# Optimization experiments

Hardware: AMD Instinct MI355X
Metric: run time of the kernel (lower is better)

Reference implementation:

```python
import jax, jax.numpy as jnp
import numpy as np

N = 1024          # nodes per atom and per input graph / barycenter
K = 8             # num_atoms
OT_LAYERS = 3     # proximal-point outer iterations inside fgwd
SINKHORN_LAYERS = 3
GWB_LAYERS = 2    # barycenter alternating-optimization iterations
PROX_BETA = 0.1   # proximal / entropic regularization strength
EPS = 1e-16


def fgwd(Gs, ps, Gb, pb):
    """Gromov-Wasserstein distance via proximal point + Sinkhorn.
    Gs:(ns,ns), ps:(ns,1), Gb:(nb,nb), pb:(nb,1). Returns (d, T) with T:(ns,nb).
    Square-loss GW cost: c(T) = f1(Gs) ps 1^T + 1 (f2(Gb) pb)^T - 2 Gs T Gb^T."""
    ns, nb = Gs.shape[0], Gb.shape[0]
    cost_st = ((Gs * Gs) @ ps) + ((Gb * Gb) @ pb).T  # (ns,1)+(1,nb) -> (ns,nb)
    T0 = ps @ pb.T  # independent-coupling init

    def ot_step(T, _):
        cost = cost_st - 2.0 * (Gs @ T @ Gb.T)
        kernel = jnp.exp(-cost / PROX_BETA) * T  # proximal-point kernel

        def sink(carry, _):
            a, b = carry
            b = pb / (kernel.T @ a + EPS)
            a = ps / (kernel @ b + EPS)
            return (a, b), None

        (a, b), _ = jax.lax.scan(sink, (ps, pb), None, length=SINKHORN_LAYERS)
        return (a * kernel) * b.T, None

    T, _ = jax.lax.scan(ot_step, T0, None, length=OT_LAYERS)
    cost = cost_st - 2.0 * (Gs @ T @ Gb.T)
    d = jnp.sum(cost * T)
    return d, T


def setup_inputs() -> dict:
    key = jax.random.key(0)
    k1, k2, k3 = jax.random.split(key, 3)
    Gm = jax.random.uniform(k1, (N, N), jnp.float32)          # input graph (sigmoid-range adjacency)
    pm = jnp.ones((N, 1), jnp.float32) / N                    # uniform node distribution
    atoms_presig = jax.random.normal(k2, (K, N, N), jnp.float32)  # pre-sigmoid atom params
    probs = jnp.ones((K, N, 1), jnp.float32) / N              # uniform atom distributions
    weights = jax.nn.softmax(jax.random.normal(k3, (K,), jnp.float32))  # output_weights
    return {"Gm": Gm, "pm": pm, "atoms_presig": atoms_presig, "probs": probs,
            "weights": weights}


def reference(Gm, pm, atoms_presig, probs, weights):
    Gk = jax.nn.sigmoid(atoms_presig)              # output_atoms: (K,N,N)
    G_bary, pb = Gm, pm                            # init_mode=0 -> barycenter init from input M
    fgwd_v = jax.vmap(fgwd, in_axes=(0, 0, None, None))
    denom = pb @ pb.T                              # pb pb^T normalizer
    for _ in range(GWB_LAYERS):
        _, trans = fgwd_v(Gk, probs, G_bary, pb)   # trans: (K,N,N)
        # comp_fgwb: sum_k w_k * T_k^T G_k T_k / (pb pb^T)
        GT = jnp.einsum('knm,kmj->knj', Gk, trans)
        G_bary = jnp.einsum('k,kni,knj->ij', weights, trans, GT) / denom
    d_fgw, _ = fgwd(Gm, pm, G_bary, pb)
    return d_fgw, G_bary
```

## Files before the change

### kernel.cpp

```cpp
#include <hip/hip_runtime.h>
#include <math.h>

#define N_   1024
#define K_   8
#define OTL  3
#define SKL  3
#define GWBL 2
#define INVB 10.0f
#define EPSV 1e-16f
#define INVN (1.0f / 1024.0f)
#define NN   ((size_t)N_ * N_)
#define KN   (K_ * N_)

typedef __attribute__((ext_vector_type(8))) short short8;
typedef __attribute__((ext_vector_type(4))) float f32x4;
typedef unsigned short bfu;

__device__ __forceinline__ float b2f(bfu u) {
    unsigned x = ((unsigned)u) << 16;
    return __builtin_bit_cast(float, x);
}
__device__ __forceinline__ bfu f2b(float f) {
    unsigned u = __builtin_bit_cast(unsigned, f);
    unsigned r = u + 0x7fffu + ((u >> 16) & 1u);
    return (bfu)(r >> 16);
}

template<int EPI>
__global__ __launch_bounds__(256, 2)
void bgemm_k(const bfu* __restrict__ A, const bfu* __restrict__ B,
             void* __restrict__ Cp, size_t sA, size_t sB, size_t sC,
             const float* __restrict__ rv, const float* __restrict__ cv,
             const float* __restrict__ wts, float* __restrict__ rs) {
    __shared__ bfu As[2][128 * 32];
    __shared__ bfu Bs[2][128 * 32];

    const int z  = blockIdx.x;
    const int bm = blockIdx.y * 128, bn = blockIdx.z * 128;
    const int tid = threadIdx.x;
    const int lane = tid & 63, wv = tid >> 6;
    const int wr = wv >> 1, wc = wv & 1;

    if (EPI == 0) {
        if (rs && blockIdx.y == 0 && blockIdx.z == 0) {
            const float4 zf = {0.f, 0.f, 0.f, 0.f};
            #pragma unroll
            for (int b = 0; b < 3; ++b)
                *(float4*)&rs[b * KN + z * N_ + tid * 4] = zf;
        }
    }

    const bfu* Az = A + (size_t)z * sA;
    const bfu* Bz = B + (size_t)z * sB;

    const int sr = tid >> 2;
    const int sk = (tid & 3) * 8;
    const int fr = lane & 15;
    const int ks = (lane >> 4) * 8;

    f32x4 acc[4][4];
    #pragma unroll
    for (int i = 0; i < 4; i++)
        #pragma unroll
        for (int j = 0; j < 4; j++) acc[i][j] = (f32x4)0.f;

    for (int k0 = 0; k0 < N_; k0 += 64) {
        __syncthreads();
        #pragma unroll
        for (int sg = 0; sg < 2; ++sg) {
            #pragma unroll
            for (int h = 0; h < 2; ++h) {
                const int row = sr + h * 64;
                const bfu* ga = Az + (size_t)(bm + row) * N_ + k0 + sg * 32 + sk;
                const bfu* gb = Bz + (size_t)(bn + row) * N_ + k0 + sg * 32 + sk;
                __builtin_amdgcn_global_load_lds(
                    (const __attribute__((address_space(1))) unsigned int*)ga,
                    (__attribute__((address_space(3))) unsigned int*)&As[sg][row * 32 + sk],
                    16, 0, 0);
                __builtin_amdgcn_global_load_lds(
                    (const __attribute__((address_space(1))) unsigned int*)gb,
                    (__attribute__((address_space(3))) unsigned int*)&Bs[sg][row * 32 + sk],
                    16, 0, 0);
            }
        }
        __syncthreads();

        #pragma unroll
        for (int sg = 0; sg < 2; ++sg) {
            short8 af[4], bf[4];
            #pragma unroll
            for (int mi = 0; mi < 4; ++mi)
                af[mi] = *(const short8*)&As[sg][(wr * 64 + mi * 16 + fr) * 32 + ks];
            #pragma unroll
            for (int ni = 0; ni < 4; ++ni)
                bf[ni] = *(const short8*)&Bs[sg][(wc * 64 + ni * 16 + fr) * 32 + ks];
            #pragma unroll
            for (int mi = 0; mi < 4; ++mi)
                #pragma unroll
                for (int ni = 0; ni < 4; ++ni)
                    acc[mi][ni] = __builtin_amdgcn_mfma_f32_16x16x32_bf16(
                        af[mi], bf[ni], acc[mi][ni], 0, 0, 0);
        }
    }

    const int r0 = bm + wr * 64, c0 = bn + wc * 64;
    const int rq = (lane >> 4) * 4;

    if (EPI == 1) {
        bfu* Cz = (bfu*)Cp + (size_t)z * sC;
        const float w = wts[z];
        #pragma unroll
        for (int mi = 0; mi < 4; ++mi)
            #pragma unroll
            for (int ni = 0; ni < 4; ++ni)
                #pragma unroll
                for (int q = 0; q < 4; ++q)
                    Cz[(size_t)(r0 + mi * 16 + rq + q) * N_ + c0 + ni * 16 + fr]
                        = f2b(w * acc[mi][ni][q]);
    } else if (EPI == 0) {
        bfu* Cz = (bfu*)Cp + (size_t)z * sC;
        #pragma unroll
        for (int mi = 0; mi < 4; ++mi)
            #pragma unroll
            for (int ni = 0; ni < 4; ++ni)
                #pragma unroll
                for (int q = 0; q < 4; ++q)
                    Cz[(size_t)(r0 + mi * 16 + rq + q) * N_ + c0 + ni * 16 + fr]
                        = f2b(acc[mi][ni][q]);
    } else {
        bfu* Cz = (bfu*)Cp + (size_t)z * sC;
        const float* rvz = rv + z * N_;
        float rsum[4][4];
        #pragma unroll
        for (int mi = 0; mi < 4; ++mi)
            #pragma unroll
            for (int q = 0; q < 4; ++q) rsum[mi][q] = 0.f;
        #pragma unroll
        for (int mi = 0; mi < 4; ++mi)
            #pragma unroll
            for (int ni = 0; ni < 4; ++ni)
                #pragma unroll
                for (int q = 0; q < 4; ++q) {
                    const int row = r0 + mi * 16 + rq + q;
                    const int col = c0 + ni * 16 + fr;
                    const float cost = rvz[col] + cv[row] - 2.f * acc[mi][ni][q];
                    const float t = b2f(Cz[(size_t)row * N_ + col]);
                    const bfu tn = f2b(expf(-cost * INVB) * t);
                    Cz[(size_t)row * N_ + col] = tn;
                    rsum[mi][q] += b2f(tn);
                }
        #pragma unroll
        for (int mi = 0; mi < 4; ++mi)
            #pragma unroll
            for (int q = 0; q < 4; ++q) {
                float v = rsum[mi][q];
                v += __shfl_xor(v, 1);
                v += __shfl_xor(v, 2);
                v += __shfl_xor(v, 4);
                v += __shfl_xor(v, 8);
                if (fr == 0)
                    atomicAdd(&rs[z * N_ + r0 + mi * 16 + rq + q], v);
            }
    }
}

template<int EPI>
__global__ __launch_bounds__(256, 2)
void gemm64_k(const bfu* __restrict__ A, const bfu* __restrict__ B,
              void* __restrict__ Cp,
              const float* __restrict__ rv, const float* __restrict__ cv,
              float* __restrict__ rs, float* __restrict__ dout) {
    __shared__ bfu As[4][64 * 32];
    __shared__ bfu Bs[4][64 * 32];
    const int bn = blockIdx.x * 64;
    const int bm = blockIdx.y * 64;
    const int tid = threadIdx.x;
    const int lane = tid & 63, wv = tid >> 6;
    const int wr = wv >> 1, wc = wv & 1;
    const int sr = tid >> 2, sk = (tid & 3) * 8;
    const int fr = lane & 15, ks = (lane >> 4) * 8;

    if (EPI == 0) {
        if (blockIdx.x == 0 && blockIdx.y == 0) {
            if (rs) {
                const float4 zf = {0.f, 0.f, 0.f, 0.f};
                #pragma unroll
                for (int b = 0; b < 3; ++b)
                    *(float4*)&rs[b * KN + tid * 4] = zf;
            }
            if (dout && tid == 0) *dout = 0.f;
        }
    }

    f32x4 acc[2][2];
    #pragma unroll
    for (int i = 0; i < 2; i++)
        #pragma unroll
        for (int j = 0; j < 2; j++) acc[i][j] = (f32x4)0.f;

    for (int k0 = 0; k0 < N_; k0 += 128) {
        __syncthreads();
        #pragma unroll
        for (int sg = 0; sg < 4; ++sg) {
            __builtin_amdgcn_global_load_lds(
                (const __attribute__((address_space(1))) unsigned int*)
                    (A + (size_t)(bm + sr) * N_ + k0 + sg * 32 + sk),
                (__attribute__((address_space(3))) unsigned int*)&As[sg][sr * 32 + sk],
                16, 0, 0);
            __builtin_amdgcn_global_load_lds(
                (const __attribute__((address_space(1))) unsigned int*)
                    (B + (size_t)(bn + sr) * N_ + k0 + sg * 32 + sk),
                (__attribute__((address_space(3))) unsigned int*)&Bs[sg][sr * 32 + sk],
                16, 0, 0);
        }
        __syncthreads();
        #pragma unroll
        for (int sg = 0; sg < 4; ++sg) {
            short8 af[2], bf[2];
            #pragma unroll
            for (int mi = 0; mi < 2; ++mi)
                af[mi] = *(const short8*)&As[sg][(wr * 32 + mi * 16 + fr) * 32 + ks];
            #pragma unroll
            for (int ni = 0; ni < 2; ++ni)
                bf[ni] = *(const short8*)&Bs[sg][(wc * 32 + ni * 16 + fr) * 32 + ks];
            #pragma unroll
            for (int mi = 0; mi < 2; ++mi)
                #pragma unroll
                for (int ni = 0; ni < 2; ++ni)
                    acc[mi][ni] = __builtin_amdgcn_mfma_f32_16x16x32_bf16(
                        af[mi], bf[ni], acc[mi][ni], 0, 0, 0);
        }
    }

    const int r0 = bm + wr * 32, c0 = bn + wc * 32;
    const int rq = (lane >> 4) * 4;

    if (EPI == 0) {
        bfu* C = (bfu*)Cp;
        #pragma unroll
        for (int mi = 0; mi < 2; ++mi)
            #pragma unroll
            for (int ni = 0; ni < 2; ++ni)
                #pragma unroll
                for (int q = 0; q < 4; ++q)
                    C[(size_t)(r0 + mi * 16 + rq + q) * N_ + c0 + ni * 16 + fr]
                        = f2b(acc[mi][ni][q]);
    } else if (EPI == 2) {
        bfu* C = (bfu*)Cp;
        float rsum[2][4];
        #pragma unroll
        for (int mi = 0; mi < 2; ++mi)
            #pragma unroll
            for (int q = 0; q < 4; ++q) rsum[mi][q] = 0.f;
        #pragma unroll
        for (int mi = 0; mi < 2; ++mi)
            #pragma unroll
            for (int ni = 0; ni < 2; ++ni)
                #pragma unroll
                for (int q = 0; q < 4; ++q) {
                    const int row = r0 + mi * 16 + rq + q;
                    const int col = c0 + ni * 16 + fr;
                    const float cost = rv[col] + cv[row] - 2.f * acc[mi][ni][q];
                    const float t = b2f(C[(size_t)row * N_ + col]);
                    const bfu tn = f2b(expf(-cost * INVB) * t);
                    C[(size_t)row * N_ + col] = tn;
                    rsum[mi][q] += b2f(tn);
                }
        #pragma unroll
        for (int mi = 0; mi < 2; ++mi)
            #pragma unroll
            for (int q = 0; q < 4; ++q) {
                float v = rsum[mi][q];
                v += __shfl_xor(v, 1);
                v += __shfl_xor(v, 2);
                v += __shfl_xor(v, 4);
                v += __shfl_xor(v, 8);
                if (fr == 0)
                    atomicAdd(&rs[r0 + mi * 16 + rq + q], v);
            }
    } else {
        const bfu* C = (const bfu*)Cp;
        float bs = 0.f;
        #pragma unroll
        for (int mi = 0; mi < 2; ++mi)
            #pragma unroll
            for (int ni = 0; ni < 2; ++ni)
                #pragma unroll
                for (int q = 0; q < 4; ++q) {
                    const int row = r0 + mi * 16 + rq + q;
                    const int col = c0 + ni * 16 + fr;
                    bs += (rv[col] + cv[row] - 2.f * acc[mi][ni][q]) *
                          b2f(C[(size_t)row * N_ + col]);
                }
        #pragma unroll
        for (int off = 32; off; off >>= 1) bs += __shfl_down(bs, off);
        __shared__ float wred[4];
        if (lane == 0) wred[wv] = bs;
        __syncthreads();
        if (tid == 0) atomicAdd(dout, wred[0] + wred[1] + wred[2] + wred[3]);
    }
}

__global__ __launch_bounds__(256)
void prox1_k(bfu* __restrict__ Tt, const float* __restrict__ c2,
             const float* __restrict__ u, const float* __restrict__ d2,
             const float* __restrict__ w, const float* __restrict__ ps,
             const float* __restrict__ pb, float* __restrict__ bv,
             float* __restrict__ rs1, int zs, int nb) {
    const int b = blockIdx.x;
    const int z  = (nb == 8) ? (b & 7) : 0;
    const int rp = (nb == 8) ? (b >> 3) : b;
    const int tid = threadIdx.x;

    if (rp < 2) {
        const float4 zf = {0.f, 0.f, 0.f, 0.f};
        *(float4*)&rs1[rp * KN + z * N_ + tid * 4] = zf;
    }

    const int half = tid >> 7;
    const int j = rp * 2 + half;
    const int i0 = (tid & 127) * 8;
    const float d2j = d2[j], wj = w[j], pbj = pb[j];
    const float* c2z = c2 + z * zs + i0;
    const float* uz  = u  + z * zs + i0;
    const float* psz = ps + z * zs + i0;
    bfu o[8];
    float s = 0.f;
    #pragma unroll
    for (int t = 0; t < 8; ++t) {
        const float cost = c2z[t] + d2j - 2.f * uz[t] * wj;
        o[t] = f2b(expf(-cost * INVB) * psz[t] * pbj);
        s += b2f(o[t]);
    }
    *(short8*)&Tt[((size_t)z << 20) + ((size_t)j << 10) + i0] = *(short8*)o;
    #pragma unroll
    for (int off = 32; off; off >>= 1) s += __shfl_down(s, off);
    __shared__ float red[4];
    if ((tid & 63) == 0) red[tid >> 6] = s;
    __syncthreads();
    if ((tid & 127) == 0)
        bv[z * N_ + j] = pbj / ((red[half * 2] + red[half * 2 + 1]) * INVN + EPSV);
}

template<int NB>
__global__ __launch_bounds__(256)
void redprox_k(const bfu* __restrict__ part, bfu* __restrict__ Gbt,
               float* __restrict__ d2out, float* __restrict__ wout,
               float* __restrict__ out1,
               const float* __restrict__ c2, const float* __restrict__ u,
               bfu* __restrict__ Tt, float* __restrict__ bv,
               float* __restrict__ rs12) {
    const int tid = threadIdx.x;
    if (blockIdx.x < 16) {
        const float4 zf = {0.f, 0.f, 0.f, 0.f};
        *(float4*)&rs12[blockIdx.x * 1024 + tid * 4] = zf;
    }
    __shared__ float red[8];
    __shared__ float bc[2];
    #pragma unroll
    for (int rep = 0; rep < 2; ++rep) {
        const int row = blockIdx.x + rep * 512;
        const size_t idx = (size_t)row * N_ + tid * 4;
        float4 s = {0.f, 0.f, 0.f, 0.f};
        #pragma unroll
        for (int sl = 0; sl < K_; ++sl) {
            bfu p[4];
            *(ulong1*)p = *(const ulong1*)&part[(size_t)sl * NN + idx];
            s.x += b2f(p[0]); s.y += b2f(p[1]);
            s.z += b2f(p[2]); s.w += b2f(p[3]);
        }
        const float sc = 1048576.f;
        s.x *= sc; s.y *= sc; s.z *= sc; s.w *= sc;
        bfu o[4];
        o[0] = f2b(s.x); o[1] = f2b(s.y); o[2] = f2b(s.z); o[3] = f2b(s.w);
        *(ulong1*)&Gbt[idx] = *(ulong1*)o;
        if (out1) {
            out1[idx + 0] = s.x; out1[idx + 1] = s.y;
            out1[idx + 2] = s.z; out1[idx + 3] = s.w;
        }
        float r2 = s.x * s.x + s.y * s.y + s.z * s.z + s.w * s.w;
        float r1 = s.x + s.y + s.z + s.w;
        #pragma unroll
        for (int off = 32; off; off >>= 1) {
            r2 += __shfl_down(r2, off);
            r1 += __shfl_down(r1, off);
        }
        if ((tid & 63) == 0) {
            red[(tid >> 6) * 2]     = r2;
            red[(tid >> 6) * 2 + 1] = r1;
        }
        __syncthreads();
        if (tid == 0) {
            const float d2j = (red[0] + red[2] + red[4] + red[6]) * INVN;
            const float wj  = (red[1] + red[3] + red[5] + red[7]) * INVN;
            d2out[row] = d2j; wout[row] = wj;
            bc[0] = d2j; bc[1] = wj;
        }
        __syncthreads();
        const float d2j = bc[0], wj = bc[1];
        const float sc2 = INVN * INVN;
        #pragma unroll
        for (int z = 0; z < NB; ++z) {
            const float4 cv4 = *(const float4*)(c2 + z * N_ + tid * 4);
            const float4 uv4 = *(const float4*)(u  + z * N_ + tid * 4);
            bfu t[4];
            t[0] = f2b(expf(-(cv4.x + d2j - 2.f * uv4.x * wj) * INVB) * sc2);
            t[1] = f2b(expf(-(cv4.y + d2j - 2.f * uv4.y * wj) * INVB) * sc2);
            t[2] = f2b(expf(-(cv4.z + d2j - 2.f * uv4.z * wj) * INVB) * sc2);
            t[3] = f2b(expf(-(cv4.w + d2j - 2.f * uv4.w * wj) * INVB) * sc2);
            *(ulong1*)&Tt[(size_t)z * NN + idx] = *(ulong1*)t;
            float rsum = b2f(t[0]) + b2f(t[1]) + b2f(t[2]) + b2f(t[3]);
            #pragma unroll
            for (int off = 32; off; off >>= 1) rsum += __shfl_down(rsum, off);
            if ((tid & 63) == 0) red[tid >> 6] = rsum;
            __syncthreads();
            if (tid == 0)
                bv[z * N_ + row] = INVN /
                    ((red[0] + red[1] + red[2] + red[3]) * INVN + EPSV);
            __syncthreads();
        }
    }
}

template<int NB, int BSRC, int TUPD>
__global__ __launch_bounds__(1024)
void sinka_k(bfu* __restrict__ Tt, const float* __restrict__ bvin,
             const float* __restrict__ rsin, const float* __restrict__ ps,
             int pstr, float* __restrict__ rsnext) {
    constexpr int CPB = (NB == 8) ? 32 : 8;
    constexpr int RG  = 1024 / CPB;
    constexpr int RPG = N_ / RG;
    int z, cb;
    if (NB == 8) { z = blockIdx.x & 7; cb = blockIdx.x >> 3; }
    else         { z = 0;              cb = blockIdx.x; }
    const int tid = threadIdx.x;
    const int cl = tid % CPB, rg = tid / CPB;
    const int i = cb * CPB + cl;
    const int zN = z * N_;
    bfu* Tz = Tt + (size_t)z * NN;

    __shared__ float bvs[1024];
    __shared__ float red[1024];
    __shared__ float avs[CPB];
    if (BSRC == 0)      bvs[tid] = bvin[zN + tid];
    else if (BSRC == 1) bvs[tid] = INVN / (rsin[zN + tid] * INVN + EPSV);
    else                bvs[tid] = INVN / (rsin[zN + tid] + EPSV);
    __syncthreads();

    float s = 0.f;
    const int j0 = rg * RPG;
    #pragma unroll 8
    for (int j = j0; j < j0 + RPG; ++j)
        s += b2f(Tz[(size_t)j * N_ + i]) * bvs[j];
    red[tid] = s;
    __syncthreads();
    #pragma unroll
    for (int h = RG / 2; h > 0; h >>= 1) {
        if (rg < h) red[rg * CPB + cl] += red[(rg + h) * CPB + cl];
        __syncthreads();
    }
    const float avi = ps[z * pstr + i] / (red[cl] + EPSV);

    if (TUPD) {
        for (int j = j0; j < j0 + RPG; ++j) {
            const size_t o = (size_t)j * N_ + i;
            Tz[o] = f2b(b2f(Tz[o]) * avi * bvs[j]);
        }
    } else {
        if (rg == 0) avs[cl] = avi;
        __syncthreads();
        const bfu* Tr = Tz + (size_t)tid * N_ + cb * CPB;
        float v = 0.f;
        #pragma unroll
        for (int q8 = 0; q8 < CPB; q8 += 8) {
            bfu t[8];
            *(short8*)t = *(const short8*)&Tr[q8];
            #pragma unroll
            for (int q = 0; q < 8; ++q) v += b2f(t[q]) * avs[q8 + q];
        }
        atomicAdd(&rsnext[zN + tid], v);
    }
}

__global__ void prep_k(const float* __restrict__ atoms, const float* __restrict__ Gm,
                       bfu* __restrict__ Gkt, bfu* __restrict__ Gmt,
                       float* __restrict__ Gk2ps, float* __restrict__ Gku,
                       float* __restrict__ Gm2pm, float* __restrict__ Gmu) {
    const int z = blockIdx.y;
    const int sig = (z < 8);
    const float* X = sig ? atoms + (size_t)z * NN : Gm;
    bfu*  Y  = sig ? Gkt + (size_t)z * NN : Gmt;
    float* y2 = sig ? Gk2ps + z * N_ : Gm2pm;
    float* y1 = sig ? Gku + z * N_ : Gmu;
    const int wv = threadIdx.x >> 6, lane = threadIdx.x & 63;
    const int r = blockIdx.x * 4 + wv;
    const float* Xr = X + (size_t)r * N_;
    bfu* Yr = Y + (size_t)r * N_;
    float s2 = 0.f, s1 = 0.f;
    for (int c = lane * 4; c < N_; c += 256) {
        float4 v = *(const float4*)(Xr + c);
        if (sig) {
            v.x = 1.f / (1.f + expf(-v.x));
            v.y = 1.f / (1.f + expf(-v.y));
            v.z = 1.f / (1.f + expf(-v.z));
            v.w = 1.f / (1.f + expf(-v.w));
        }
        bfu o[4];
        o[0] = f2b(v.x); o[1] = f2b(v.y); o[2] = f2b(v.z); o[3] = f2b(v.w);
        *(ulong1*)&Yr[c] = *(ulong1*)o;
        s2 += v.x * v.x + v.y * v.y + v.z * v.z + v.w * v.w;
        s1 += v.x + v.y + v.z + v.w;
    }
    #pragma unroll
    for (int off = 32; off; off >>= 1) {
        s2 += __shfl_down(s2, off);
        s1 += __shfl_down(s1, off);
    }
    if (lane == 0) {
        y2[r] = s2 * INVN;
        y1[r] = s1 * INVN;
    }
}


template<int NB, int BSRC1>
static inline void sink_tail(bfu* Tt, const float* ps, int pstr,
                             float* bvec, float* rs, hipStream_t stream) {
    const dim3 ga((NB == 8) ? 256 : 128);
    float* rs1 = rs + KN;
    float* rs2 = rs + 2 * KN;
    sinka_k<NB, BSRC1, 0><<<ga, dim3(1024), 0, stream>>>(Tt, bvec, rs, ps, pstr, rs1);
    sinka_k<NB, 2, 0><<<ga, dim3(1024), 0, stream>>>(Tt, nullptr, rs1, ps, pstr, rs2);
    sinka_k<NB, 2, 1><<<ga, dim3(1024), 0, stream>>>(Tt, nullptr, rs2, ps, pstr, nullptr);
}

extern "C" void kernel_launch(void* const* d_in, const int* in_sizes, int n_in,
                              void* d_out, int out_size, void* d_ws, size_t ws_size,
                              hipStream_t stream) {
    const float* Gm    = (const float*)d_in[0];
    const float* pm    = (const float*)d_in[1];
    const float* atoms = (const float*)d_in[2];
    const float* probs = (const float*)d_in[3];
    const float* wts   = (const float*)d_in[4];
    float* out = (float*)d_out;

    char* base = (char*)d_ws;
    bfu*   Gkt  = (bfu*)base;                    base += K_ * NN * 2;
    bfu*   Tt   = (bfu*)base;                    base += K_ * NN * 2;
    bfu*   M    = (bfu*)base;                    base += K_ * NN * 2;
    bfu*   part = (bfu*)base;                    base += K_ * NN * 2;
    bfu*   Gbt  = (bfu*)base;                    base += NN * 2;
    bfu*   Gmt  = (bfu*)base;                    base += NN * 2;
    float* Gk2ps = (float*)base;                 base += KN * 4;
    float* Gku   = (float*)base;                 base += KN * 4;
    float* Gm2pm = (float*)base;                 base += N_ * 4;
    float* Gmu   = (float*)base;                 base += N_ * 4;
    float* Gb2pb = (float*)base;                 base += N_ * 4;
    float* Gbw   = (float*)base;                 base += N_ * 4;
    float* bvec  = (float*)base;                 base += KN * 4;
    float* rs    = (float*)base;                 base += 3 * KN * 4;

    const dim3 blk(256);
    const dim3 g8(8, 8, 8);
    const dim3 g64(16, 16);

    prep_k<<<dim3(256, 9), blk, 0, stream>>>(atoms, Gm, Gkt, Gmt,
                                             Gk2ps, Gku, Gm2pm, Gmu);

    for (int it = 0; it < GWBL; ++it) {
        const bfu*   GbtU = it ? Gbt : Gmt;
        const float* d2U  = it ? Gb2pb : Gm2pm;

        if (it == 0)
            prox1_k<<<512 * K_, blk, 0, stream>>>(Tt, Gk2ps, Gku, Gm2pm, Gmu,
                                                  probs, pm, bvec, rs + KN, N_, K_);
        sink_tail<K_, 0>(Tt, probs, N_, bvec, rs, stream);
        for (int ot = 1; ot < OTL; ++ot) {
            bgemm_k<0><<<g8, blk, 0, stream>>>(Gkt, Tt, M, NN, NN, NN,
                nullptr, nullptr, nullptr, rs);
            bgemm_k<2><<<g8, blk, 0, stream>>>(GbtU, M, Tt, 0, NN, NN,
                Gk2ps, d2U, nullptr, rs);
            sink_tail<K_, 1>(Tt, probs, N_, bvec, rs, stream);
        }
        bgemm_k<0><<<g8, blk, 0, stream>>>(Tt, Gkt, M, NN, NN, NN,
            nullptr, nullptr, nullptr, nullptr);
        bgemm_k<1><<<g8, blk, 0, stream>>>(Tt, M, part, NN, NN, NN,
            nullptr, nullptr, wts, nullptr);
        if (it == 0)
            redprox_k<8><<<512, blk, 0, stream>>>(part, Gbt, Gb2pb, Gbw,
                nullptr, Gk2ps, Gku, Tt, bvec, rs + KN);
        else
            redprox_k<1><<<512, blk, 0, stream>>>(part, Gbt, Gb2pb, Gbw,
                out + 1, Gm2pm, Gmu, Tt, bvec, rs + KN);
    }

    sink_tail<1, 0>(Tt, pm, 0, bvec, rs, stream);
    for (int ot = 1; ot < OTL; ++ot) {
        gemm64_k<0><<<g64, blk, 0, stream>>>(Gmt, Tt, M,
            nullptr, nullptr, rs, nullptr);
        gemm64_k<2><<<g64, blk, 0, stream>>>(Gbt, M, Tt,
            Gm2pm, Gb2pb, rs, nullptr);
        sink_tail<1, 1>(Tt, pm, 0, bvec, rs, stream);
    }
    gemm64_k<0><<<g64, blk, 0, stream>>>(Gmt, Tt, M,
        nullptr, nullptr, nullptr, out );
    gemm64_k<3><<<g64, blk, 0, stream>>>(Gbt, M, Tt,
        Gm2pm, Gb2pb, nullptr, out);
}
```

Before: 622.4 us.

## Restructure Sinkhorn column kernel to hold tile in registers with vector loads

Rewrites the Sinkhorn a-update kernel so each thread loads 8 contiguous bf16 values per row with one vector load and keeps them in registers. Column sums are reduced with wavefront shuffles instead of a multi-step shared-memory tree, and the same registers feed the transposed row-sum and the T update, so T is no longer re-read from global memory. For the batched case the column block shrinks from 32 to 16 and the grid doubles to 512 blocks. The aim is to cut strided scalar global loads, reloads of T and barrier count, at the cost of more registers per thread.

```diff
diff --git a/kernel.cpp b/kernel.cpp
--- a/kernel.cpp
+++ b/kernel.cpp
@@ -427,58 +427,89 @@
 void sinka_k(bfu* __restrict__ Tt, const float* __restrict__ bvin,
              const float* __restrict__ rsin, const float* __restrict__ ps,
              int pstr, float* __restrict__ rsnext) {
-    constexpr int CPB = (NB == 8) ? 32 : 8;
-    constexpr int RG  = 1024 / CPB;
-    constexpr int RPG = N_ / RG;
+    constexpr int CPB  = (NB == 8) ? 16 : 8;
+    constexpr int RPT  = (NB == 8) ? 2 : 1;
+    constexpr int FIRST = (NB == 8) ? 2 : 1;
     int z, cb;
     if (NB == 8) { z = blockIdx.x & 7; cb = blockIdx.x >> 3; }
     else         { z = 0;              cb = blockIdx.x; }
     const int tid = threadIdx.x;
-    const int cl = tid % CPB, rg = tid / CPB;
-    const int i = cb * CPB + cl;
+    const int vc = (NB == 8) ? (tid & 1) : 0;
+    const int rg = (NB == 8) ? (tid >> 1) : tid;
+    const int c0 = cb * CPB + vc * 8;
     const int zN = z * N_;
     bfu* Tz = Tt + (size_t)z * NN;
 
     __shared__ float bvs[1024];
-    __shared__ float red[1024];
+    __shared__ float red[16][CPB];
     __shared__ float avs[CPB];
     if (BSRC == 0)      bvs[tid] = bvin[zN + tid];
     else if (BSRC == 1) bvs[tid] = INVN / (rsin[zN + tid] * INVN + EPSV);
     else                bvs[tid] = INVN / (rsin[zN + tid] + EPSV);
     __syncthreads();
 
-    float s = 0.f;
-    const int j0 = rg * RPG;
-    #pragma unroll 8
-    for (int j = j0; j < j0 + RPG; ++j)
-        s += b2f(Tz[(size_t)j * N_ + i]) * bvs[j];
-    red[tid] = s;
+    bfu tr[RPT][8];
+    float rowb[RPT];
+    float sc[8];
+    #pragma unroll
+    for (int q = 0; q < 8; ++q) sc[q] = 0.f;
+    #pragma unroll
+    for (int r = 0; r < RPT; ++r) {
+        const int j = rg * RPT + r;
+        rowb[r] = bvs[j];
+        *(short8*)tr[r] = *(const short8*)&Tz[(size_t)j * N_ + c0];
+        #pragma unroll
+        for (int q = 0; q < 8; ++q) sc[q] += b2f(tr[r][q]) * rowb[r];
+    }
+    #pragma unroll
+    for (int off = FIRST; off < 64; off <<= 1)
+        #pragma unroll
+        for (int q = 0; q < 8; ++q) sc[q] += __shfl_down(sc[q], off);
+    const int wv = tid >> 6, lane = tid & 63;
+    if (lane < FIRST) {
+        const int cbase = (NB == 8) ? lane * 8 : 0;
+        #pragma unroll
+        for (int q = 0; q < 8; ++q) red[wv][cbase + q] = sc[q];
+    }
     __syncthreads();
-    #pragma unroll
-    for (int h = RG / 2; h > 0; h >>= 1) {
-        if (rg < h) red[rg * CPB + cl] += red[(rg + h) * CPB + cl];
-        __syncthreads();
-    }
-    const float avi = ps[z * pstr + i] / (red[cl] + EPSV);
+    if (tid < CPB) {
+        float s = 0.f;
+        #pragma unroll
+        for (int w = 0; w < 16; ++w) s += red[w][tid];
+        avs[tid] = ps[z * pstr + cb * CPB + tid] / (s + EPSV);
+    }
+    __syncthreads();
 
     if (TUPD) {
-        for (int j = j0; j < j0 + RPG; ++j) {
-            const size_t o = (size_t)j * N_ + i;
-            Tz[o] = f2b(b2f(Tz[o]) * avi * bvs[j]);
+        #pragma unroll
+        for (int r = 0; r < RPT; ++r) {
+            const int j = rg * RPT + r;
+            bfu o[8];
+            #pragma unroll
+            for (int q = 0; q < 8; ++q)
+                o[q] = f2b(b2f(tr[r][q]) * avs[vc * 8 + q] * rowb[r]);
+            *(short8*)&Tz[(size_t)j * N_ + c0] = *(short8*)o;
         }
     } else {
-        if (rg == 0) avs[cl] = avi;
-        __syncthreads();
-        const bfu* Tr = Tz + (size_t)tid * N_ + cb * CPB;
-        float v = 0.f;
-        #pragma unroll
-        for (int q8 = 0; q8 < CPB; q8 += 8) {
-            bfu t[8];
-            *(short8*)t = *(const short8*)&Tr[q8];
-            #pragma unroll
-            for (int q = 0; q < 8; ++q) v += b2f(t[q]) * avs[q8 + q];
-        }
-        atomicAdd(&rsnext[zN + tid], v);
+        float v[RPT];
+        #pragma unroll
+        for (int r = 0; r < RPT; ++r) {
+            v[r] = 0.f;
+            #pragma unroll
+            for (int q = 0; q < 8; ++q)
+                v[r] += b2f(tr[r][q]) * avs[vc * 8 + q];
+        }
+        if (NB == 8) {
+            #pragma unroll
+            for (int r = 0; r < RPT; ++r) v[r] += __shfl_xor(v[r], 1);
+            if (vc == 0) {
+                #pragma unroll
+                for (int r = 0; r < RPT; ++r)
+                    atomicAdd(&rsnext[zN + rg * RPT + r], v[r]);
+            }
+        } else {
+            atomicAdd(&rsnext[zN + tid], v[0]);
+        }
     }
 }
 
@@ -526,7 +557,7 @@
 template<int NB, int BSRC1>
 static inline void sink_tail(bfu* Tt, const float* ps, int pstr,
                              float* bvec, float* rs, hipStream_t stream) {
-    const dim3 ga((NB == 8) ? 256 : 128);
+    const dim3 ga((NB == 8) ? 512 : 128);
     float* rs1 = rs + KN;
     float* rs2 = rs + 2 * KN;
     sinka_k<NB, BSRC1, 0><<<ga, dim3(1024), 0, stream>>>(Tt, bvec, rs, ps, pstr, rs1);
```

After: 647.5 us. 4.0% more time.
